# Performance work log

Measured on AMD Instinct MI355X. Metric: run time of the kernel, lower is better.

The kernel has to match this reference:

```python
import jax, jax.numpy as jnp
import numpy as np

HIDDEN = 2048
N_HEADS = 16
N_KV_HEADS = 4
HEAD_DIM = HIDDEN // N_HEADS  # 128
BATCH = 2
SEQ = 2048


def setup_inputs() -> dict:
    key = jax.random.key(0)
    ks = jax.random.split(key, 10)
    s = 0.02
    return {
        "hidden_states": jax.random.normal(ks[0], (BATCH, SEQ, HIDDEN), jnp.float32),
        "attention_mask": jnp.ones((BATCH, SEQ), jnp.int32),
        # weights stored [in, out] so y = x @ W + b (transpose of torch layout)
        "Wq": jax.random.normal(ks[1], (HIDDEN, N_HEADS * HEAD_DIM), jnp.float32) * s,
        "bq": jnp.zeros((N_HEADS * HEAD_DIM,), jnp.float32),
        "Wk": jax.random.normal(ks[2], (HIDDEN, N_KV_HEADS * HEAD_DIM), jnp.float32) * s,
        "bk": jnp.zeros((N_KV_HEADS * HEAD_DIM,), jnp.float32),
        "Wv": jax.random.normal(ks[3], (HIDDEN, N_KV_HEADS * HEAD_DIM), jnp.float32) * s,
        "bv": jnp.zeros((N_KV_HEADS * HEAD_DIM,), jnp.float32),
        "Wo": jax.random.normal(ks[4], (N_HEADS * HEAD_DIM, HIDDEN), jnp.float32) * s,
        "bo": jnp.zeros((HIDDEN,), jnp.float32),
    }


def reference(hidden_states, attention_mask, Wq, bq, Wk, bk, Wv, bv, Wo, bo):
    B, S, _ = hidden_states.shape
    q = hidden_states @ Wq + bq  # [B,S,H*D]
    k = hidden_states @ Wk + bk  # [B,S,Hkv*D]
    v = hidden_states @ Wv + bv

    q = q.reshape(B, S, N_HEADS, HEAD_DIM).transpose(0, 2, 1, 3)      # [B,H,S,D]
    k = k.reshape(B, S, N_KV_HEADS, HEAD_DIM).transpose(0, 2, 1, 3)   # [B,Hkv,S,D]
    v = v.reshape(B, S, N_KV_HEADS, HEAD_DIM).transpose(0, 2, 1, 3)

    # GQA: repeat_interleave along head dim (head h uses kv head h // groups)
    groups = N_HEADS // N_KV_HEADS
    k = jnp.repeat(k, groups, axis=1)  # [B,H,S,D]
    v = jnp.repeat(v, groups, axis=1)

    scale = 1.0 / np.sqrt(HEAD_DIM)
    scores = jnp.einsum('bhqd,bhkd->bhqk', q, k) * scale  # [B,H,S,S]

    causal = jnp.tril(jnp.ones((S, S), bool))              # True = keep
    keep = causal[None, None, :, :] & (attention_mask[:, None, None, :] != 0)
    scores = jnp.where(keep, scores, -jnp.inf)

    attn = jax.nn.softmax(scores.astype(jnp.float32), axis=-1).astype(q.dtype)
    out = jnp.einsum('bhqk,bhkd->bhqd', attn, v)            # [B,H,S,D]
    out = out.transpose(0, 2, 1, 3).reshape(B, S, N_HEADS * HEAD_DIM)
    return out @ Wo + bo
```

## Files before the change

kernel.cpp:

```cpp
#include <hip/hip_runtime.h>
#include <hip/hip_bf16.h>


typedef unsigned short u16;
typedef unsigned long long u64;
typedef __attribute__((ext_vector_type(8))) short short8;
typedef __attribute__((ext_vector_type(4))) float f32x4;
typedef __attribute__((ext_vector_type(4))) unsigned uint4v;

#define BATCH 2
#define SEQ 2048
#define HIDDEN 2048
#define NH 16
#define NKV 4
#define HD 128
#define QKV_N 3072
#define MROWS 4096

__device__ inline u16 f2bf(float f) {
    __hip_bfloat16 h = __float2bfloat16(f);
    return __builtin_bit_cast(u16, h);
}

__device__ inline void async_copy16(const u16* g, u16* lds_base) {
    __builtin_amdgcn_global_load_lds(
        (const __attribute__((address_space(1))) void*)g,
        (__attribute__((address_space(3))) void*)lds_base, 16, 0, 0);
}

#define PREP_CONV   4096
#define PREP_WQ     (PREP_CONV + 1024)
#define PREP_WK     (PREP_WQ + 256)
#define PREP_WV     (PREP_WK + 256)
#define PREP_WO     (PREP_WV + 1024)
#define PREP_BIAS   (PREP_WO + 12)
#define PREP_TOTAL  (PREP_BIAS + 1)

__device__ inline void prep_transpose64(const float* __restrict__ src, u16* __restrict__ dst,
                                        int N, int sub, float (*tl)[69]) {
    int nx = N >> 6;
    int bx = sub % nx, by = sub / nx;
    int n0 = bx * 64, k0 = by * 64;
    int t = threadIdx.x;
    int rr = t >> 4, cc = (t & 15) * 4;
#pragma unroll
    for (int j = 0; j < 4; ++j) {
        float4 v = *(const float4*)(src + (size_t)(k0 + rr + 16 * j) * N + n0 + cc);
        int k = rr + 16 * j;
        tl[cc + 0][k] = v.x;
        tl[cc + 1][k] = v.y;
        tl[cc + 2][k] = v.z;
        tl[cc + 3][k] = v.w;
    }
    __syncthreads();
    int n = t >> 2;
#pragma unroll
    for (int j = 0; j < 2; ++j) {
        int kk = (t & 3) * 8 + 32 * j;
        short8 o8;
#pragma unroll
        for (int i = 0; i < 8; ++i) o8[i] = (short)f2bf(tl[n][kk + i]);
        *(short8*)(dst + (size_t)(n0 + n) * HIDDEN + k0 + kk) = o8;
    }
}

__global__ __launch_bounds__(256)
void prep(const float* __restrict__ hidden, u16* __restrict__ xb,
          const float* __restrict__ Wq, const float* __restrict__ Wk,
          const float* __restrict__ Wv, const float* __restrict__ Wo,
          u16* __restrict__ wqkvT, u16* __restrict__ woT,
          const float* __restrict__ bq, const float* __restrict__ bk,
          const float* __restrict__ bv, float* __restrict__ bqkv,
          const int* __restrict__ am, u64* __restrict__ mp) {
    __shared__ float tl[64][69];
    int bid = blockIdx.x;
    if (bid < PREP_CONV) {
        int i = (bid * 256 + threadIdx.x) * 8;
        float4 v0 = *(const float4*)(hidden + i);
        float4 v1 = *(const float4*)(hidden + i + 4);
        short8 o8;
        o8[0] = (short)f2bf(v0.x); o8[1] = (short)f2bf(v0.y);
        o8[2] = (short)f2bf(v0.z); o8[3] = (short)f2bf(v0.w);
        o8[4] = (short)f2bf(v1.x); o8[5] = (short)f2bf(v1.y);
        o8[6] = (short)f2bf(v1.z); o8[7] = (short)f2bf(v1.w);
        *(short8*)(xb + i) = o8;
    } else if (bid < PREP_WQ) {
        prep_transpose64(Wq, wqkvT, 2048, bid - PREP_CONV, tl);
    } else if (bid < PREP_WK) {
        prep_transpose64(Wk, wqkvT + (size_t)2048 * HIDDEN, 512, bid - PREP_WQ, tl);
    } else if (bid < PREP_WV) {
        prep_transpose64(Wv, wqkvT + (size_t)2560 * HIDDEN, 512, bid - PREP_WK, tl);
    } else if (bid < PREP_WO) {
        prep_transpose64(Wo, woT, 2048, bid - PREP_WV, tl);
    } else if (bid < PREP_BIAS) {
        int i = (bid - PREP_WO) * 256 + threadIdx.x;
        if (i < QKV_N)
            bqkv[i] = (i < 2048) ? bq[i] : ((i < 2560) ? bk[i - 2048] : bv[i - 2560]);
    } else {
        int i = threadIdx.x;
        if (i < BATCH * SEQ / 64) {
            const int* a = am + i * 64;
            u64 m = 0;
#pragma unroll
            for (int j = 0; j < 64; j += 4) {
                int4 v = *(const int4*)(a + j);
                m |= ((u64)(v.x != 0) << j) | ((u64)(v.y != 0) << (j + 1)) |
                     ((u64)(v.z != 0) << (j + 2)) | ((u64)(v.w != 0) << (j + 3));
            }
            mp[i] = m;
        }
    }
}

__global__ __launch_bounds__(256)
void vt_from_qkv(const u16* __restrict__ qkv, u16* __restrict__ vt) {
    __shared__ u16 tl[64][72];
    int b = blockIdx.z >> 2, kvh = blockIdx.z & 3;
    int s0 = blockIdx.x * 64, d0 = blockIdx.y * 64;
    int t = threadIdx.x;
    int sr = t >> 2, ch = t & 3;
#pragma unroll
    for (int j = 0; j < 2; ++j) {
        int dd = (ch + 4 * j) * 8;
        short8 v = *(const short8*)(qkv + (size_t)(b * SEQ + s0 + sr) * QKV_N +
                                    2560 + kvh * HD + d0 + dd);
#pragma unroll
        for (int i = 0; i < 8; ++i) tl[dd + i][sr] = (u16)v[i];
    }
    __syncthreads();
#pragma unroll
    for (int j = 0; j < 2; ++j) {
        int ss = (ch + 4 * j) * 8;
        short8 o;
#pragma unroll
        for (int i = 0; i < 8; ++i) o[i] = (short)tl[sr][ss + i];
        *(short8*)(vt + (size_t)((b * NKV + kvh) * HD + d0 + sr) * SEQ + s0 + ss) = o;
    }
}

template <bool OUT_BF16>
__global__ __launch_bounds__(512, 2)
void gemm_bf16_256(const u16* __restrict__ A, const u16* __restrict__ BT,
                   const float* __restrict__ bias, void* __restrict__ outp,
                   int M, int N, int K) {
    __shared__ __align__(16) u16 smem[2][2][256][64];
    const int t = threadIdx.x, w = t >> 6, lane = t & 63;
    const int quad = lane >> 4, l16 = lane & 15;
    const int wm = w >> 2, wn = w & 3;
    const int bm0 = blockIdx.y * 256, bn0 = blockIdx.x * 256;
    const int lrow = lane >> 3;
    const int lchk = (lane & 7) ^ lrow;
    const int NT = K >> 6;

    f32x4 acc[8][4];
#pragma unroll
    for (int i = 0; i < 8; i++)
#pragma unroll
        for (int j = 0; j < 4; j++) acc[i][j] = (f32x4){0.f, 0.f, 0.f, 0.f};

    const u16* gA = A + (size_t)bm0 * K;
    const u16* gB = BT + (size_t)bn0 * K;

    auto stage = [&](int buf, int op, int h, int k0) {
        const u16* gb = op ? gB : gA;
#pragma unroll
        for (int l = 0; l < 2; ++l) {
            int rb = h * 128 + w * 16 + l * 8;
            async_copy16(gb + (size_t)(rb + lrow) * K + k0 + lchk * 8,
                         &smem[buf][op][rb][0]);
        }
    };
    auto readA = [&](short8 (&aq)[4][2], int buf, int mh) {
#pragma unroll
        for (int mt = 0; mt < 4; ++mt) {
            int row = mh * 128 + mt * 32 + wm * 16 + l16;
            int swz = row & 7;
#pragma unroll
            for (int kk = 0; kk < 2; ++kk) {
                int chunk = ((kk << 2) | quad) ^ swz;
                aq[mt][kk] = *(const short8*)(&smem[buf][0][row][chunk << 3]);
            }
        }
    };
    auto readB = [&](short8 (&bq)[2][2], int buf, int nh) {
#pragma unroll
        for (int nt = 0; nt < 2; ++nt) {
            int row = nh * 128 + nt * 64 + wn * 16 + l16;
            int swz = row & 7;
#pragma unroll
            for (int kk = 0; kk < 2; ++kk) {
                int chunk = ((kk << 2) | quad) ^ swz;
                bq[nt][kk] = *(const short8*)(&smem[buf][1][row][chunk << 3]);
            }
        }
    };
    auto mmaQ = [&](short8 (&aq)[4][2], short8 (&bq)[2][2], int mh, int nh) {
        __builtin_amdgcn_s_setprio(1);
#pragma unroll
        for (int mt = 0; mt < 4; ++mt)
#pragma unroll
            for (int nt = 0; nt < 2; ++nt)
#pragma unroll
                for (int kk = 0; kk < 2; ++kk)
                    acc[mh * 4 + mt][nh * 2 + nt] = __builtin_amdgcn_mfma_f32_16x16x32_bf16(
                        aq[mt][kk], bq[nt][kk], acc[mh * 4 + mt][nh * 2 + nt], 0, 0, 0);
        __builtin_amdgcn_s_setprio(0);
    };

    stage(0, 0, 0, 0); stage(0, 1, 0, 0); stage(0, 1, 1, 0); stage(0, 0, 1, 0);
    asm volatile("s_waitcnt vmcnt(4)" ::: "memory");
    __builtin_amdgcn_s_barrier();

    short8 aq[4][2], b0[2][2], b1[2][2];
    for (int tt = 0; tt < NT - 1; ++tt) {
        const int cur = tt & 1, nxt = cur ^ 1, k1 = (tt + 1) << 6;
        readA(aq, cur, 0); readB(b0, cur, 0);
        stage(nxt, 0, 0, k1);
        mmaQ(aq, b0, 0, 0);
        asm volatile("s_waitcnt vmcnt(4)" ::: "memory");
        __builtin_amdgcn_s_barrier();
        readB(b1, cur, 1);
        stage(nxt, 1, 0, k1);
        mmaQ(aq, b1, 0, 1);
        asm volatile("s_waitcnt vmcnt(4)" ::: "memory");
        __builtin_amdgcn_s_barrier();
        readA(aq, cur, 1);
        stage(nxt, 1, 1, k1);
        mmaQ(aq, b1, 1, 1);
        asm volatile("s_waitcnt vmcnt(6)" ::: "memory");
        __builtin_amdgcn_s_barrier();
        stage(nxt, 0, 1, k1);
        mmaQ(aq, b0, 1, 0);
        asm volatile("s_waitcnt vmcnt(4)" ::: "memory");
        __builtin_amdgcn_s_barrier();
    }
    asm volatile("s_waitcnt vmcnt(0)" ::: "memory");
    __builtin_amdgcn_s_barrier();
    {
        const int cur = (NT - 1) & 1;
        readA(aq, cur, 0); readB(b0, cur, 0);
        mmaQ(aq, b0, 0, 0);
        readB(b1, cur, 1);
        mmaQ(aq, b1, 0, 1);
        readA(aq, cur, 1);
        mmaQ(aq, b1, 1, 1);
        mmaQ(aq, b0, 1, 0);
    }

#pragma unroll
    for (int nt = 0; nt < 4; ++nt) {
        int col = bn0 + nt * 64 + wn * 16 + l16;
        float bcol = bias[col];
#pragma unroll
        for (int mt = 0; mt < 8; ++mt) {
#pragma unroll
            for (int r = 0; r < 4; ++r) {
                int row = bm0 + mt * 32 + wm * 16 + quad * 4 + r;
                float v = acc[mt][nt][r] + bcol;
                if constexpr (OUT_BF16)
                    ((u16*)outp)[(size_t)row * N + col] = f2bf(v);
                else
                    ((float*)outp)[(size_t)row * N + col] = v;
            }
        }
    }
}

__global__ __launch_bounds__(512, 2)
void gemm_bf16_128x256(const u16* __restrict__ A, const u16* __restrict__ BT,
                       const float* __restrict__ bias, float* __restrict__ outp,
                       int M, int N, int K) {
    __shared__ __align__(16) u16 sA[2][128][64];
    __shared__ __align__(16) u16 sB[2][256][64];
    const int t = threadIdx.x, w = t >> 6, lane = t & 63;
    const int quad = lane >> 4, l16 = lane & 15;
    const int wm = w >> 2, wn = w & 3;
    const int bm0 = blockIdx.y * 128, bn0 = blockIdx.x * 256;
    const int lrow = lane >> 3;
    const int lchk = (lane & 7) ^ lrow;
    const int NT = K >> 6;

    f32x4 acc[4][4];
#pragma unroll
    for (int i = 0; i < 4; i++)
#pragma unroll
        for (int j = 0; j < 4; j++) acc[i][j] = (f32x4){0.f, 0.f, 0.f, 0.f};

    const u16* gA = A + (size_t)bm0 * K;
    const u16* gB = BT + (size_t)bn0 * K;

    auto stageA = [&](int buf, int k0) {
#pragma unroll
        for (int l = 0; l < 2; ++l) {
            int rb = w * 16 + l * 8;
            async_copy16(gA + (size_t)(rb + lrow) * K + k0 + lchk * 8, &sA[buf][rb][0]);
        }
    };
    auto stageB = [&](int buf, int h, int k0) {
#pragma unroll
        for (int l = 0; l < 2; ++l) {
            int rb = h * 128 + w * 16 + l * 8;
            async_copy16(gB + (size_t)(rb + lrow) * K + k0 + lchk * 8, &sB[buf][rb][0]);
        }
    };
    auto readA = [&](short8 (&aq)[4][2], int buf) {
#pragma unroll
        for (int mt = 0; mt < 4; ++mt) {
            int row = wm * 64 + mt * 16 + l16;
            int swz = row & 7;
#pragma unroll
            for (int kk = 0; kk < 2; ++kk) {
                int chunk = ((kk << 2) | quad) ^ swz;
                aq[mt][kk] = *(const short8*)(&sA[buf][row][chunk << 3]);
            }
        }
    };
    auto readB = [&](short8 (&bq)[2][2], int buf, int nh) {
#pragma unroll
        for (int nt = 0; nt < 2; ++nt) {
            int row = nh * 128 + nt * 64 + wn * 16 + l16;
            int swz = row & 7;
#pragma unroll
            for (int kk = 0; kk < 2; ++kk) {
                int chunk = ((kk << 2) | quad) ^ swz;
                bq[nt][kk] = *(const short8*)(&sB[buf][row][chunk << 3]);
            }
        }
    };
    auto mmaH = [&](short8 (&aq)[4][2], short8 (&bq)[2][2], int nh) {
        __builtin_amdgcn_s_setprio(1);
#pragma unroll
        for (int mt = 0; mt < 4; ++mt)
#pragma unroll
            for (int nt = 0; nt < 2; ++nt)
#pragma unroll
                for (int kk = 0; kk < 2; ++kk)
                    acc[mt][nh * 2 + nt] = __builtin_amdgcn_mfma_f32_16x16x32_bf16(
                        aq[mt][kk], bq[nt][kk], acc[mt][nh * 2 + nt], 0, 0, 0);
        __builtin_amdgcn_s_setprio(0);
    };

    stageA(0, 0); stageB(0, 0, 0); stageB(0, 1, 0);
    asm volatile("s_waitcnt vmcnt(2)" ::: "memory");
    __builtin_amdgcn_s_barrier();

    short8 aq[4][2], b0[2][2], b1[2][2];
    for (int tt = 0; tt < NT - 1; ++tt) {
        const int cur = tt & 1, nxt = cur ^ 1, k1 = (tt + 1) << 6;
        readA(aq, cur); readB(b0, cur, 0);
        stageA(nxt, k1); stageB(nxt, 0, k1);
        mmaH(aq, b0, 0);
        asm volatile("s_waitcnt vmcnt(4)" ::: "memory");
        __builtin_amdgcn_s_barrier();
        readB(b1, cur, 1);
        stageB(nxt, 1, k1);
        mmaH(aq, b1, 1);
        asm volatile("s_waitcnt vmcnt(2)" ::: "memory");
        __builtin_amdgcn_s_barrier();
    }
    asm volatile("s_waitcnt vmcnt(0)" ::: "memory");
    __builtin_amdgcn_s_barrier();
    {
        const int cur = (NT - 1) & 1;
        readA(aq, cur); readB(b0, cur, 0);
        mmaH(aq, b0, 0);
        readB(b1, cur, 1);
        mmaH(aq, b1, 1);
    }

#pragma unroll
    for (int j = 0; j < 4; ++j) {
        int col = bn0 + j * 64 + wn * 16 + l16;
        float bcol = bias[col];
#pragma unroll
        for (int mt = 0; mt < 4; ++mt) {
#pragma unroll
            for (int r = 0; r < 4; ++r) {
                int row = bm0 + wm * 64 + mt * 16 + quad * 4 + r;
                outp[(size_t)row * N + col] = acc[mt][j][r] + bcol;
            }
        }
    }
}

__global__ __launch_bounds__(512, 4)
void flash_attn(const u16* __restrict__ qkv, const u16* __restrict__ vt,
                const u64* __restrict__ mp, u16* __restrict__ attn) {
    __shared__ __align__(16) u16 Ks[64][136];
    __shared__ __align__(16) u16 Vs[128][72];
    int t = threadIdx.x, w = t >> 6, lane = t & 63, quad = lane >> 4, l16 = lane & 15;
    int bx = blockIdx.x, b = blockIdx.z;
    int qt = b ? ((int)gridDim.x - 1 - bx) : bx;
    int h = blockIdx.y, kvh = h >> 2;
    int q_row0 = qt * 128 + w * 16;

    const u16* qrow = qkv + (size_t)(b * SEQ + q_row0 + l16) * QKV_N + h * HD;
    short8 qf[4];
#pragma unroll
    for (int c = 0; c < 4; c++) qf[c] = *(const short8*)(qrow + c * 32 + quad * 8);

    f32x4 o[8];
#pragma unroll
    for (int dt = 0; dt < 8; dt++) o[dt] = (f32x4){0.f, 0.f, 0.f, 0.f};
    float lpart = 0.f;

    const float scale2 = 0.12751743f;
    const float C2 = 14.4269504f;

    const u16* kgb = qkv + (size_t)(b * SEQ) * QKV_N + 2048 + kvh * HD;
    const u16* vgb = vt + (size_t)((b * NKV + kvh) * HD) * SEQ;
    const u64* mpb = mp + b * (SEQ / 64);

    int kr = t >> 4, kc = (t & 15) * 8;
    int vr = t >> 3, vc = (t & 7) * 8;
    int kb_end = (qt + 1) * 128;

    short8 k0p, k1p, v0p, v1p;
    {
        k0p = *(const short8*)(kgb + (size_t)kr * QKV_N + kc);
        k1p = *(const short8*)(kgb + (size_t)(kr + 32) * QKV_N + kc);
        v0p = *(const short8*)(vgb + (size_t)vr * SEQ + vc);
        v1p = *(const short8*)(vgb + (size_t)(vr + 64) * SEQ + vc);
    }

    for (int kb = 0; kb < kb_end; kb += 64) {
        __syncthreads();
        *(short8*)(&Ks[kr][kc]) = k0p;
        *(short8*)(&Ks[kr + 32][kc]) = k1p;
        *(short8*)(&Vs[vr][vc]) = v0p;
        *(short8*)(&Vs[vr + 64][vc]) = v1p;
        __syncthreads();
        if (kb + 64 < kb_end) {
            const u16* kg = kgb + (size_t)(kb + 64) * QKV_N;
            const u16* vg = vgb + kb + 64;
            k0p = *(const short8*)(kg + (size_t)kr * QKV_N + kc);
            k1p = *(const short8*)(kg + (size_t)(kr + 32) * QKV_N + kc);
            v0p = *(const short8*)(vg + (size_t)vr * SEQ + vc);
            v1p = *(const short8*)(vg + (size_t)(vr + 64) * SEQ + vc);
        }
        if (kb > q_row0 + 15) continue;

        u64 mk = mpb[kb >> 6];

        f32x4 sc[4];
#pragma unroll
        for (int nt = 0; nt < 4; nt++) sc[nt] = (f32x4){0.f, 0.f, 0.f, 0.f};
        __builtin_amdgcn_s_setprio(1);
#pragma unroll
        for (int c = 0; c < 4; c++) {
#pragma unroll
            for (int nt = 0; nt < 4; nt++) {
                short8 kf = *(const short8*)(&Ks[nt * 16 + l16][c * 32 + quad * 8]);
                sc[nt] = __builtin_amdgcn_mfma_f32_16x16x32_bf16(kf, qf[c], sc[nt], 0, 0, 0);
            }
        }
        __builtin_amdgcn_s_setprio(0);

        short8 vf0a[4];
#pragma unroll
        for (int dt = 0; dt < 4; dt++)
            vf0a[dt] = *(const short8*)(&Vs[dt * 16 + l16][quad * 8]);

        float p[4][4];
        if (mk == ~0ull && kb + 63 <= q_row0) {
#pragma unroll
            for (int nt = 0; nt < 4; nt++)
#pragma unroll
                for (int r = 0; r < 4; r++)
                    p[nt][r] = __builtin_exp2f(__builtin_fmaf(sc[nt][r], scale2, -C2));
        } else {
            int limit = q_row0 + l16 - kb;
#pragma unroll
            for (int nt = 0; nt < 4; nt++) {
                unsigned nib = (unsigned)(mk >> (nt * 16 + quad * 4));
#pragma unroll
                for (int r = 0; r < 4; r++) {
                    int bp = nt * 16 + quad * 4 + r;
                    bool ok = ((nib >> r) & 1u) && (bp <= limit);
                    float v = ok ? sc[nt][r] : -INFINITY;
                    p[nt][r] = __builtin_exp2f(__builtin_fmaf(v, scale2, -C2));
                }
            }
        }
        lpart += ((p[0][0] + p[0][1]) + (p[0][2] + p[0][3])) +
                 ((p[1][0] + p[1][1]) + (p[1][2] + p[1][3])) +
                 ((p[2][0] + p[2][1]) + (p[2][2] + p[2][3])) +
                 ((p[3][0] + p[3][1]) + (p[3][2] + p[3][3]));

        unsigned A0, A1, B0, B1, C0, C1, E0, E1;
        asm("v_cvt_pk_bf16_f32 %0, %1, %2" : "=v"(A0) : "v"(p[0][0]), "v"(p[0][1]));
        asm("v_cvt_pk_bf16_f32 %0, %1, %2" : "=v"(A1) : "v"(p[0][2]), "v"(p[0][3]));
        asm("v_cvt_pk_bf16_f32 %0, %1, %2" : "=v"(B0) : "v"(p[1][0]), "v"(p[1][1]));
        asm("v_cvt_pk_bf16_f32 %0, %1, %2" : "=v"(B1) : "v"(p[1][2]), "v"(p[1][3]));
        asm("v_cvt_pk_bf16_f32 %0, %1, %2" : "=v"(C0) : "v"(p[2][0]), "v"(p[2][1]));
        asm("v_cvt_pk_bf16_f32 %0, %1, %2" : "=v"(C1) : "v"(p[2][2]), "v"(p[2][3]));
        asm("v_cvt_pk_bf16_f32 %0, %1, %2" : "=v"(E0) : "v"(p[3][0]), "v"(p[3][1]));
        asm("v_cvt_pk_bf16_f32 %0, %1, %2" : "=v"(E1) : "v"(p[3][2]), "v"(p[3][3]));
        asm("v_permlane32_swap_b32 %0, %1" : "+v"(A0), "+v"(B0));
        asm("v_permlane16_swap_b32 %0, %1" : "+v"(A0), "+v"(B0));
        asm("v_permlane32_swap_b32 %0, %1" : "+v"(A1), "+v"(B1));
        asm("v_permlane16_swap_b32 %0, %1" : "+v"(A1), "+v"(B1));
        asm("v_permlane32_swap_b32 %0, %1" : "+v"(C0), "+v"(E0));
        asm("v_permlane16_swap_b32 %0, %1" : "+v"(C0), "+v"(E0));
        asm("v_permlane32_swap_b32 %0, %1" : "+v"(C1), "+v"(E1));
        asm("v_permlane16_swap_b32 %0, %1" : "+v"(C1), "+v"(E1));
        short8 pf0 = __builtin_bit_cast(short8, (uint4v){A0, A1, B0, B1});
        short8 pf1 = __builtin_bit_cast(short8, (uint4v){C0, C1, E0, E1});

        __builtin_amdgcn_s_setprio(1);
#pragma unroll
        for (int dt = 0; dt < 4; dt++)
            o[dt] = __builtin_amdgcn_mfma_f32_16x16x32_bf16(pf0, vf0a[dt], o[dt], 0, 0, 0);
#pragma unroll
        for (int dt = 4; dt < 8; dt++) {
            short8 vf0 = *(const short8*)(&Vs[dt * 16 + l16][quad * 8]);
            o[dt] = __builtin_amdgcn_mfma_f32_16x16x32_bf16(pf0, vf0, o[dt], 0, 0, 0);
        }
#pragma unroll
        for (int dt = 0; dt < 8; dt++) {
            short8 vf1 = *(const short8*)(&Vs[dt * 16 + l16][32 + quad * 8]);
            o[dt] = __builtin_amdgcn_mfma_f32_16x16x32_bf16(pf1, vf1, o[dt], 0, 0, 0);
        }
        __builtin_amdgcn_s_setprio(0);
    }
    float l = lpart;
    l += __shfl_xor(l, 16, 64);
    l += __shfl_xor(l, 32, 64);
    float invq[4];
#pragma unroll
    for (int r = 0; r < 4; r++) {
        float lr = __shfl(l, quad * 4 + r, 16);
        invq[r] = lr > 0.f ? 1.f / lr : 0.f;
    }
    size_t obase = (size_t)(b * SEQ + q_row0) * HIDDEN + h * HD;
#pragma unroll
    for (int dt = 0; dt < 8; dt++)
#pragma unroll
        for (int r = 0; r < 4; r++)
            attn[obase + (size_t)(quad * 4 + r) * HIDDEN + dt * 16 + l16] =
                f2bf(o[dt][r] * invq[r]);
}

extern "C" void kernel_launch(void* const* d_in, const int* in_sizes, int n_in,
                              void* d_out, int out_size, void* d_ws, size_t ws_size,
                              hipStream_t stream) {
    const float* hidden = (const float*)d_in[0];
    const int* amask   = (const int*)d_in[1];
    const float* Wq = (const float*)d_in[2];
    const float* bq = (const float*)d_in[3];
    const float* Wk = (const float*)d_in[4];
    const float* bk = (const float*)d_in[5];
    const float* Wv = (const float*)d_in[6];
    const float* bv = (const float*)d_in[7];
    const float* Wo = (const float*)d_in[8];
    const float* bo = (const float*)d_in[9];
    float* out = (float*)d_out;

    char* ws = (char*)d_ws;
    u16* xb     = (u16*)ws;  ws += (size_t)MROWS * HIDDEN * 2;
    u16* wqkvT  = (u16*)ws;  ws += (size_t)QKV_N * HIDDEN * 2;
    u16* woT    = (u16*)ws;  ws += (size_t)HIDDEN * HIDDEN * 2;
    float* bqkv = (float*)ws; ws += (size_t)QKV_N * 4;
    u64* mpk    = (u64*)ws;  ws += (size_t)(MROWS / 64) * 8;
    u16* qkv    = (u16*)ws;  ws += (size_t)MROWS * QKV_N * 2;
    u16* vt     = (u16*)ws;  ws += (size_t)BATCH * NKV * HD * SEQ * 2;
    u16* attn   = (u16*)ws;  ws += (size_t)MROWS * HIDDEN * 2;

    prep<<<dim3(PREP_TOTAL), dim3(256), 0, stream>>>(
        hidden, xb, Wq, Wk, Wv, Wo, wqkvT, woT, bq, bk, bv, bqkv, amask, mpk);

    gemm_bf16_256<true><<<dim3(QKV_N / 256, MROWS / 256), dim3(512), 0, stream>>>(
        xb, wqkvT, bqkv, qkv, MROWS, QKV_N, HIDDEN);

    vt_from_qkv<<<dim3(SEQ / 64, HD / 64, BATCH * NKV), dim3(256), 0, stream>>>(qkv, vt);

    flash_attn<<<dim3(SEQ / 128, NH, BATCH), dim3(512), 0, stream>>>(qkv, vt, mpk, attn);

    gemm_bf16_128x256<<<dim3(HIDDEN / 256, MROWS / 128), dim3(512), 0, stream>>>(
        attn, woT, bo, out, MROWS, HIDDEN, HIDDEN);
}
```

Before: 278.2 us.

## Double-buffer flash attention K/V tiles with async global-to-LDS copies

Replaces the register-staged K/V prefetch (load into registers, then store to LDS between two barriers) with direct asynchronous global-to-LDS copies into a double-buffered shared memory tile. The next tile is copied into the other buffer while the current one is being consumed, so only one barrier per iteration remains. Copy addressing follows the padded LDS row layout, with a few lanes and waves handling the remainder chunks. This doubles the LDS footprint of the attention kernel, which may reduce occupancy, and pad lanes load into the padding columns.

```diff
diff --git a/kernel.cpp b/kernel.cpp
--- a/kernel.cpp
+++ b/kernel.cpp
@@ -386,8 +386,8 @@
 __global__ __launch_bounds__(512, 4)
 void flash_attn(const u16* __restrict__ qkv, const u16* __restrict__ vt,
                 const u64* __restrict__ mp, u16* __restrict__ attn) {
-    __shared__ __align__(16) u16 Ks[64][136];
-    __shared__ __align__(16) u16 Vs[128][72];
+    __shared__ __align__(16) u16 Ks[2][64][136];
+    __shared__ __align__(16) u16 Vs[2][128][72];
     int t = threadIdx.x, w = t >> 6, lane = t & 63, quad = lane >> 4, l16 = lane & 15;
     int bx = blockIdx.x, b = blockIdx.z;
     int qt = b ? ((int)gridDim.x - 1 - bx) : bx;
@@ -411,32 +411,54 @@
     const u16* vgb = vt + (size_t)((b * NKV + kvh) * HD) * SEQ;
     const u64* mpb = mp + b * (SEQ / 64);
 
-    int kr = t >> 4, kc = (t & 15) * 8;
-    int vr = t >> 3, vc = (t & 7) * 8;
+    const int kI0 = w, kI1 = w + 8, kI2 = 16;
+    const int vI0 = w, vI1 = w + 8, vI2 = 16 + w;
+    const bool hasK2 = (w == 0), hasV2 = (w < 2);
+    auto kaddr = [&](int I) -> const u16* {
+        int c = I * 64 + lane;
+        int row = c / 17, col = (c % 17) * 8;
+        if (col >= 128) col = 0;
+        return kgb + (size_t)row * QKV_N + col;
+    };
+    auto vaddr = [&](int I) -> const u16* {
+        int c = I * 64 + lane;
+        int row = c / 9, col = (c % 9) * 8;
+        if (col >= 64) col = 0;
+        return vgb + (size_t)row * SEQ + col;
+    };
+    const u16 *ka0 = kaddr(kI0), *ka1 = kaddr(kI1), *ka2 = kaddr(kI2);
+    const u16 *va0 = vaddr(vI0), *va1 = vaddr(vI1), *va2 = vaddr(vI2);
+    const size_t kStep = (size_t)64 * QKV_N;
     int kb_end = (qt + 1) * 128;
 
-    short8 k0p, k1p, v0p, v1p;
     {
-        k0p = *(const short8*)(kgb + (size_t)kr * QKV_N + kc);
-        k1p = *(const short8*)(kgb + (size_t)(kr + 32) * QKV_N + kc);
-        v0p = *(const short8*)(vgb + (size_t)vr * SEQ + vc);
-        v1p = *(const short8*)(vgb + (size_t)(vr + 64) * SEQ + vc);
-    }
-
-    for (int kb = 0; kb < kb_end; kb += 64) {
-        __syncthreads();
-        *(short8*)(&Ks[kr][kc]) = k0p;
-        *(short8*)(&Ks[kr + 32][kc]) = k1p;
-        *(short8*)(&Vs[vr][vc]) = v0p;
-        *(short8*)(&Vs[vr + 64][vc]) = v1p;
-        __syncthreads();
+        u16* kb0 = &Ks[0][0][0];
+        u16* vb0 = &Vs[0][0][0];
+        async_copy16(ka0, kb0 + kI0 * 512);
+        async_copy16(ka1, kb0 + kI1 * 512);
+        if (hasK2) async_copy16(ka2, kb0 + kI2 * 512);
+        async_copy16(va0, vb0 + vI0 * 512);
+        async_copy16(va1, vb0 + vI1 * 512);
+        if (hasV2) async_copy16(va2, vb0 + vI2 * 512);
+        ka0 += kStep; ka1 += kStep; ka2 += kStep;
+        va0 += 64; va1 += 64; va2 += 64;
+    }
+
+    int cur = 0;
+    for (int kb = 0; kb < kb_end; kb += 64, cur ^= 1) {
+        asm volatile("s_waitcnt vmcnt(0)" ::: "memory");
+        __builtin_amdgcn_s_barrier();
         if (kb + 64 < kb_end) {
-            const u16* kg = kgb + (size_t)(kb + 64) * QKV_N;
-            const u16* vg = vgb + kb + 64;
-            k0p = *(const short8*)(kg + (size_t)kr * QKV_N + kc);
-            k1p = *(const short8*)(kg + (size_t)(kr + 32) * QKV_N + kc);
-            v0p = *(const short8*)(vg + (size_t)vr * SEQ + vc);
-            v1p = *(const short8*)(vg + (size_t)(vr + 64) * SEQ + vc);
+            u16* kbn = &Ks[cur ^ 1][0][0];
+            u16* vbn = &Vs[cur ^ 1][0][0];
+            async_copy16(ka0, kbn + kI0 * 512);
+            async_copy16(ka1, kbn + kI1 * 512);
+            if (hasK2) async_copy16(ka2, kbn + kI2 * 512);
+            async_copy16(va0, vbn + vI0 * 512);
+            async_copy16(va1, vbn + vI1 * 512);
+            if (hasV2) async_copy16(va2, vbn + vI2 * 512);
+            ka0 += kStep; ka1 += kStep; ka2 += kStep;
+            va0 += 64; va1 += 64; va2 += 64;
         }
         if (kb > q_row0 + 15) continue;
 
@@ -450,7 +472,7 @@
         for (int c = 0; c < 4; c++) {
 #pragma unroll
             for (int nt = 0; nt < 4; nt++) {
-                short8 kf = *(const short8*)(&Ks[nt * 16 + l16][c * 32 + quad * 8]);
+                short8 kf = *(const short8*)(&Ks[cur][nt * 16 + l16][c * 32 + quad * 8]);
                 sc[nt] = __builtin_amdgcn_mfma_f32_16x16x32_bf16(kf, qf[c], sc[nt], 0, 0, 0);
             }
         }
@@ -459,7 +481,7 @@
         short8 vf0a[4];
 #pragma unroll
         for (int dt = 0; dt < 4; dt++)
-            vf0a[dt] = *(const short8*)(&Vs[dt * 16 + l16][quad * 8]);
+            vf0a[dt] = *(const short8*)(&Vs[cur][dt * 16 + l16][quad * 8]);
 
         float p[4][4];
         if (mk == ~0ull && kb + 63 <= q_row0) {
@@ -513,12 +535,12 @@
             o[dt] = __builtin_amdgcn_mfma_f32_16x16x32_bf16(pf0, vf0a[dt], o[dt], 0, 0, 0);
 #pragma unroll
         for (int dt = 4; dt < 8; dt++) {
-            short8 vf0 = *(const short8*)(&Vs[dt * 16 + l16][quad * 8]);
+            short8 vf0 = *(const short8*)(&Vs[cur][dt * 16 + l16][quad * 8]);
             o[dt] = __builtin_amdgcn_mfma_f32_16x16x32_bf16(pf0, vf0, o[dt], 0, 0, 0);
         }
 #pragma unroll
         for (int dt = 0; dt < 8; dt++) {
-            short8 vf1 = *(const short8*)(&Vs[dt * 16 + l16][32 + quad * 8]);
+            short8 vf1 = *(const short8*)(&Vs[cur][dt * 16 + l16][32 + quad * 8]);
             o[dt] = __builtin_amdgcn_mfma_f32_16x16x32_bf16(pf1, vf1, o[dt], 0, 0, 0);
         }
         __builtin_amdgcn_s_setprio(0);
```

New measurement: 282.6 us. About the same (+1.6%).

## Double-buffer K/V shared tiles in flash attention to halve barriers

Applied to the files above, without the earlier changes.

Flash attention's K/V shared-memory tiles become double-buffered. Each iteration writes the next tile from registers into the other buffer and issues global loads two tiles ahead, so only one barrier per iteration is needed instead of two. This is meant to cut synchronisation stalls and overlap LDS staging with MFMA compute. In exchange it doubles the kernel's LDS footprint (about 70 KB per block), which could limit occupancy under the 512-thread, 4-block launch bounds.

```diff
diff --git a/kernel.cpp b/kernel.cpp
--- a/kernel.cpp
+++ b/kernel.cpp
@@ -386,8 +386,8 @@
 __global__ __launch_bounds__(512, 4)
 void flash_attn(const u16* __restrict__ qkv, const u16* __restrict__ vt,
                 const u64* __restrict__ mp, u16* __restrict__ attn) {
-    __shared__ __align__(16) u16 Ks[64][136];
-    __shared__ __align__(16) u16 Vs[128][72];
+    __shared__ __align__(16) u16 Ks[2][64][136];
+    __shared__ __align__(16) u16 Vs[2][128][72];
     int t = threadIdx.x, w = t >> 6, lane = t & 63, quad = lane >> 4, l16 = lane & 15;
     int bx = blockIdx.x, b = blockIdx.z;
     int qt = b ? ((int)gridDim.x - 1 - bx) : bx;
@@ -413,115 +413,121 @@
 
     int kr = t >> 4, kc = (t & 15) * 8;
     int vr = t >> 3, vc = (t & 7) * 8;
-    int kb_end = (qt + 1) * 128;
+    const int NTK = (qt + 1) * 2;
 
     short8 k0p, k1p, v0p, v1p;
-    {
-        k0p = *(const short8*)(kgb + (size_t)kr * QKV_N + kc);
-        k1p = *(const short8*)(kgb + (size_t)(kr + 32) * QKV_N + kc);
-        v0p = *(const short8*)(vgb + (size_t)vr * SEQ + vc);
-        v1p = *(const short8*)(vgb + (size_t)(vr + 64) * SEQ + vc);
-    }
-
-    for (int kb = 0; kb < kb_end; kb += 64) {
+    auto loadregs = [&](int tile) {
+        const u16* kg = kgb + (size_t)(tile * 64) * QKV_N;
+        const u16* vg = vgb + tile * 64;
+        k0p = *(const short8*)(kg + (size_t)kr * QKV_N + kc);
+        k1p = *(const short8*)(kg + (size_t)(kr + 32) * QKV_N + kc);
+        v0p = *(const short8*)(vg + (size_t)vr * SEQ + vc);
+        v1p = *(const short8*)(vg + (size_t)(vr + 64) * SEQ + vc);
+    };
+    auto writebuf = [&](int buf) {
+        *(short8*)(&Ks[buf][kr][kc]) = k0p;
+        *(short8*)(&Ks[buf][kr + 32][kc]) = k1p;
+        *(short8*)(&Vs[buf][vr][vc]) = v0p;
+        *(short8*)(&Vs[buf][vr + 64][vc]) = v1p;
+    };
+
+    loadregs(0);
+    writebuf(0);
+    loadregs(1);
+    __syncthreads();
+
+    for (int tt = 0; tt < NTK; ++tt) {
+        const int cur = tt & 1;
+        if (tt + 1 < NTK) {
+            writebuf(cur ^ 1);
+            if (tt + 2 < NTK) loadregs(tt + 2);
+        }
+        int kb = tt * 64;
+        if (kb <= q_row0 + 15) {
+            u64 mk = mpb[kb >> 6];
+
+            f32x4 sc[4];
+#pragma unroll
+            for (int nt = 0; nt < 4; nt++) sc[nt] = (f32x4){0.f, 0.f, 0.f, 0.f};
+            __builtin_amdgcn_s_setprio(1);
+#pragma unroll
+            for (int c = 0; c < 4; c++) {
+#pragma unroll
+                for (int nt = 0; nt < 4; nt++) {
+                    short8 kf = *(const short8*)(&Ks[cur][nt * 16 + l16][c * 32 + quad * 8]);
+                    sc[nt] = __builtin_amdgcn_mfma_f32_16x16x32_bf16(kf, qf[c], sc[nt], 0, 0, 0);
+                }
+            }
+            __builtin_amdgcn_s_setprio(0);
+
+            short8 vf0a[4];
+#pragma unroll
+            for (int dt = 0; dt < 4; dt++)
+                vf0a[dt] = *(const short8*)(&Vs[cur][dt * 16 + l16][quad * 8]);
+
+            float p[4][4];
+            if (mk == ~0ull && kb + 63 <= q_row0) {
+#pragma unroll
+                for (int nt = 0; nt < 4; nt++)
+#pragma unroll
+                    for (int r = 0; r < 4; r++)
+                        p[nt][r] = __builtin_exp2f(__builtin_fmaf(sc[nt][r], scale2, -C2));
+            } else {
+                int limit = q_row0 + l16 - kb;
+#pragma unroll
+                for (int nt = 0; nt < 4; nt++) {
+                    unsigned nib = (unsigned)(mk >> (nt * 16 + quad * 4));
+#pragma unroll
+                    for (int r = 0; r < 4; r++) {
+                        int bp = nt * 16 + quad * 4 + r;
+                        bool ok = ((nib >> r) & 1u) && (bp <= limit);
+                        float v = ok ? sc[nt][r] : -INFINITY;
+                        p[nt][r] = __builtin_exp2f(__builtin_fmaf(v, scale2, -C2));
+                    }
+                }
+            }
+            lpart += ((p[0][0] + p[0][1]) + (p[0][2] + p[0][3])) +
+                     ((p[1][0] + p[1][1]) + (p[1][2] + p[1][3])) +
+                     ((p[2][0] + p[2][1]) + (p[2][2] + p[2][3])) +
+                     ((p[3][0] + p[3][1]) + (p[3][2] + p[3][3]));
+
+            unsigned A0, A1, B0, B1, C0, C1, E0, E1;
+            asm("v_cvt_pk_bf16_f32 %0, %1, %2" : "=v"(A0) : "v"(p[0][0]), "v"(p[0][1]));
+            asm("v_cvt_pk_bf16_f32 %0, %1, %2" : "=v"(A1) : "v"(p[0][2]), "v"(p[0][3]));
+            asm("v_cvt_pk_bf16_f32 %0, %1, %2" : "=v"(B0) : "v"(p[1][0]), "v"(p[1][1]));
+            asm("v_cvt_pk_bf16_f32 %0, %1, %2" : "=v"(B1) : "v"(p[1][2]), "v"(p[1][3]));
+            asm("v_cvt_pk_bf16_f32 %0, %1, %2" : "=v"(C0) : "v"(p[2][0]), "v"(p[2][1]));
+            asm("v_cvt_pk_bf16_f32 %0, %1, %2" : "=v"(C1) : "v"(p[2][2]), "v"(p[2][3]));
+            asm("v_cvt_pk_bf16_f32 %0, %1, %2" : "=v"(E0) : "v"(p[3][0]), "v"(p[3][1]));
+            asm("v_cvt_pk_bf16_f32 %0, %1, %2" : "=v"(E1) : "v"(p[3][2]), "v"(p[3][3]));
+            asm("v_permlane32_swap_b32 %0, %1" : "+v"(A0), "+v"(B0));
+            asm("v_permlane16_swap_b32 %0, %1" : "+v"(A0), "+v"(B0));
+            asm("v_permlane32_swap_b32 %0, %1" : "+v"(A1), "+v"(B1));
+            asm("v_permlane16_swap_b32 %0, %1" : "+v"(A1), "+v"(B1));
+            asm("v_permlane32_swap_b32 %0, %1" : "+v"(C0), "+v"(E0));
+            asm("v_permlane16_swap_b32 %0, %1" : "+v"(C0), "+v"(E0));
+            asm("v_permlane32_swap_b32 %0, %1" : "+v"(C1), "+v"(E1));
+            asm("v_permlane16_swap_b32 %0, %1" : "+v"(C1), "+v"(E1));
+            short8 pf0 = __builtin_bit_cast(short8, (uint4v){A0, A1, B0, B1});
+            short8 pf1 = __builtin_bit_cast(short8, (uint4v){C0, C1, E0, E1});
+
+            __builtin_amdgcn_s_setprio(1);
+#pragma unroll
+            for (int dt = 0; dt < 4; dt++)
+                o[dt] = __builtin_amdgcn_mfma_f32_16x16x32_bf16(pf0, vf0a[dt], o[dt], 0, 0, 0);
+#pragma unroll
+            for (int dt = 4; dt < 8; dt++) {
+                short8 vf0 = *(const short8*)(&Vs[cur][dt * 16 + l16][quad * 8]);
+                o[dt] = __builtin_amdgcn_mfma_f32_16x16x32_bf16(pf0, vf0, o[dt], 0, 0, 0);
+            }
+#pragma unroll
+            for (int dt = 0; dt < 8; dt++) {
+                short8 vf1 = *(const short8*)(&Vs[cur][dt * 16 + l16][32 + quad * 8]);
+                o[dt] = __builtin_amdgcn_mfma_f32_16x16x32_bf16(pf1, vf1, o[dt], 0, 0, 0);
+            }
+            __builtin_amdgcn_s_setprio(0);
+        }
         __syncthreads();
-        *(short8*)(&Ks[kr][kc]) = k0p;
-        *(short8*)(&Ks[kr + 32][kc]) = k1p;
-        *(short8*)(&Vs[vr][vc]) = v0p;
-        *(short8*)(&Vs[vr + 64][vc]) = v1p;
-        __syncthreads();
-        if (kb + 64 < kb_end) {
-            const u16* kg = kgb + (size_t)(kb + 64) * QKV_N;
-            const u16* vg = vgb + kb + 64;
-            k0p = *(const short8*)(kg + (size_t)kr * QKV_N + kc);
-            k1p = *(const short8*)(kg + (size_t)(kr + 32) * QKV_N + kc);
-            v0p = *(const short8*)(vg + (size_t)vr * SEQ + vc);
-            v1p = *(const short8*)(vg + (size_t)(vr + 64) * SEQ + vc);
-        }
-        if (kb > q_row0 + 15) continue;
-
-        u64 mk = mpb[kb >> 6];
-
-        f32x4 sc[4];
-#pragma unroll
-        for (int nt = 0; nt < 4; nt++) sc[nt] = (f32x4){0.f, 0.f, 0.f, 0.f};
-        __builtin_amdgcn_s_setprio(1);
-#pragma unroll
-        for (int c = 0; c < 4; c++) {
-#pragma unroll
-            for (int nt = 0; nt < 4; nt++) {
-                short8 kf = *(const short8*)(&Ks[nt * 16 + l16][c * 32 + quad * 8]);
-                sc[nt] = __builtin_amdgcn_mfma_f32_16x16x32_bf16(kf, qf[c], sc[nt], 0, 0, 0);
-            }
-        }
-        __builtin_amdgcn_s_setprio(0);
-
-        short8 vf0a[4];
-#pragma unroll
-        for (int dt = 0; dt < 4; dt++)
-            vf0a[dt] = *(const short8*)(&Vs[dt * 16 + l16][quad * 8]);
-
-        float p[4][4];
-        if (mk == ~0ull && kb + 63 <= q_row0) {
-#pragma unroll
-            for (int nt = 0; nt < 4; nt++)
-#pragma unroll
-                for (int r = 0; r < 4; r++)
-                    p[nt][r] = __builtin_exp2f(__builtin_fmaf(sc[nt][r], scale2, -C2));
-        } else {
-            int limit = q_row0 + l16 - kb;
-#pragma unroll
-            for (int nt = 0; nt < 4; nt++) {
-                unsigned nib = (unsigned)(mk >> (nt * 16 + quad * 4));
-#pragma unroll
-                for (int r = 0; r < 4; r++) {
-                    int bp = nt * 16 + quad * 4 + r;
-                    bool ok = ((nib >> r) & 1u) && (bp <= limit);
-                    float v = ok ? sc[nt][r] : -INFINITY;
-                    p[nt][r] = __builtin_exp2f(__builtin_fmaf(v, scale2, -C2));
-                }
-            }
-        }
-        lpart += ((p[0][0] + p[0][1]) + (p[0][2] + p[0][3])) +
-                 ((p[1][0] + p[1][1]) + (p[1][2] + p[1][3])) +
-                 ((p[2][0] + p[2][1]) + (p[2][2] + p[2][3])) +
-                 ((p[3][0] + p[3][1]) + (p[3][2] + p[3][3]));
-
-        unsigned A0, A1, B0, B1, C0, C1, E0, E1;
-        asm("v_cvt_pk_bf16_f32 %0, %1, %2" : "=v"(A0) : "v"(p[0][0]), "v"(p[0][1]));
-        asm("v_cvt_pk_bf16_f32 %0, %1, %2" : "=v"(A1) : "v"(p[0][2]), "v"(p[0][3]));
-        asm("v_cvt_pk_bf16_f32 %0, %1, %2" : "=v"(B0) : "v"(p[1][0]), "v"(p[1][1]));
-        asm("v_cvt_pk_bf16_f32 %0, %1, %2" : "=v"(B1) : "v"(p[1][2]), "v"(p[1][3]));
-        asm("v_cvt_pk_bf16_f32 %0, %1, %2" : "=v"(C0) : "v"(p[2][0]), "v"(p[2][1]));
-        asm("v_cvt_pk_bf16_f32 %0, %1, %2" : "=v"(C1) : "v"(p[2][2]), "v"(p[2][3]));
-        asm("v_cvt_pk_bf16_f32 %0, %1, %2" : "=v"(E0) : "v"(p[3][0]), "v"(p[3][1]));
-        asm("v_cvt_pk_bf16_f32 %0, %1, %2" : "=v"(E1) : "v"(p[3][2]), "v"(p[3][3]));
-        asm("v_permlane32_swap_b32 %0, %1" : "+v"(A0), "+v"(B0));
-        asm("v_permlane16_swap_b32 %0, %1" : "+v"(A0), "+v"(B0));
-        asm("v_permlane32_swap_b32 %0, %1" : "+v"(A1), "+v"(B1));
-        asm("v_permlane16_swap_b32 %0, %1" : "+v"(A1), "+v"(B1));
-        asm("v_permlane32_swap_b32 %0, %1" : "+v"(C0), "+v"(E0));
-        asm("v_permlane16_swap_b32 %0, %1" : "+v"(C0), "+v"(E0));
-        asm("v_permlane32_swap_b32 %0, %1" : "+v"(C1), "+v"(E1));
-        asm("v_permlane16_swap_b32 %0, %1" : "+v"(C1), "+v"(E1));
-        short8 pf0 = __builtin_bit_cast(short8, (uint4v){A0, A1, B0, B1});
-        short8 pf1 = __builtin_bit_cast(short8, (uint4v){C0, C1, E0, E1});
-
-        __builtin_amdgcn_s_setprio(1);
-#pragma unroll
-        for (int dt = 0; dt < 4; dt++)
-            o[dt] = __builtin_amdgcn_mfma_f32_16x16x32_bf16(pf0, vf0a[dt], o[dt], 0, 0, 0);
-#pragma unroll
-        for (int dt = 4; dt < 8; dt++) {
-            short8 vf0 = *(const short8*)(&Vs[dt * 16 + l16][quad * 8]);
-            o[dt] = __builtin_amdgcn_mfma_f32_16x16x32_bf16(pf0, vf0, o[dt], 0, 0, 0);
-        }
-#pragma unroll
-        for (int dt = 0; dt < 8; dt++) {
-            short8 vf1 = *(const short8*)(&Vs[dt * 16 + l16][32 + quad * 8]);
-            o[dt] = __builtin_amdgcn_mfma_f32_16x16x32_bf16(pf1, vf1, o[dt], 0, 0, 0);
-        }
-        __builtin_amdgcn_s_setprio(0);
     }
     float l = lpart;
     l += __shfl_xor(l, 16, 64);
```

New measurement: 287.3 us. +3.3%, slower.
